# Performance work log

Hardware: AMD Instinct MI355X
Metric: run time of the kernel (lower is better)

The kernel has to match this reference:

```python
import jax, jax.numpy as jnp
import numpy as np

B, SQ, SKV = 4, 2048, 2048
INPUT_DIM, EMBED_DIM, NUM_HEADS = 1024, 1024, 16
HEAD_DIM = EMBED_DIM // NUM_HEADS


def setup_inputs() -> dict:
    key = jax.random.key(0)
    kq, kc, kwkv, kwo = jax.random.split(key, 4)
    # xavier-uniform style scale for weights
    def xavier(k, shape):
        fan_in, fan_out = shape
        lim = jnp.sqrt(6.0 / (fan_in + fan_out))
        return jax.random.uniform(k, shape, jnp.float32, -lim, lim)
    return {
        "q": jax.random.normal(kq, (B, SQ, EMBED_DIM), jnp.float32),
        "c": jax.random.normal(kc, (B, SKV, INPUT_DIM), jnp.float32),
        "W_kv": xavier(kwkv, (INPUT_DIM, 2 * EMBED_DIM)),
        "b_kv": jnp.zeros((2 * EMBED_DIM,), jnp.float32),
        "W_o": xavier(kwo, (EMBED_DIM, EMBED_DIM)),
        "b_o": jnp.zeros((EMBED_DIM,), jnp.float32),
    }


def reference(q, c, W_kv, b_kv, W_o, b_o):
    Bc, Skv, _ = c.shape
    Bq, Sq, embed_dim = q.shape
    # KV projection from context: [B, Skv, 2*embed_dim]
    kv = c @ W_kv + b_kv
    kv = kv.reshape(Bc, Skv, NUM_HEADS, 2 * HEAD_DIM).transpose(0, 2, 1, 3)  # [B,H,Skv,2*hd]
    k, v = jnp.split(kv, 2, axis=-1)  # each [B,H,Skv,hd]
    # q is pre-projected; just split into heads
    qh = q.reshape(Bq, Sq, NUM_HEADS, HEAD_DIM).transpose(0, 2, 1, 3)  # [B,H,Sq,hd]
    scale = 1.0 / jnp.sqrt(jnp.asarray(HEAD_DIM, q.dtype))
    logits = jnp.einsum("bhqd,bhkd->bhqk", qh, k) * scale  # [B,H,Sq,Skv]
    attn = jax.nn.softmax(logits, axis=-1)
    values = jnp.einsum("bhqk,bhkd->bhqd", attn, v)  # [B,H,Sq,hd]
    values = values.transpose(0, 2, 1, 3).reshape(Bc, Sq, embed_dim)
    out = values @ W_o + b_o
    return out
```

## Files before the change

### kernel.cpp

```cpp
#include <hip/hip_runtime.h>

typedef __bf16 bf16x8 __attribute__((ext_vector_type(8)));
typedef float f32x4 __attribute__((ext_vector_type(4)));
typedef unsigned short u16;
typedef unsigned short u16x4 __attribute__((ext_vector_type(4)));
typedef unsigned short u16x8 __attribute__((ext_vector_type(8)));

#define DEVFN __device__ __forceinline__

DEVFN u16 f32_to_bf16(float f) {
  unsigned int u = __float_as_uint(f);
  u += 0x7FFFu + ((u >> 16) & 1u);
  return (u16)(u >> 16);
}

DEVFN u16 f32_to_bf16_fast(float f) {
  return (u16)((__float_as_uint(f) + 0x8000u) >> 16);
}

DEVFN void load_lds16(const void* g, void* l) {
  __builtin_amdgcn_global_load_lds(
      (__attribute__((address_space(1))) void*)g,
      (__attribute__((address_space(3))) void*)l,
      16, 0, 0);
}


__global__ void cvt_c_kernel(const float* __restrict__ in, u16* __restrict__ out) {
  int i = blockIdx.x * 256 + threadIdx.x;
  const float4* p = (const float4*)in + (size_t)i * 2;
  float4 a = p[0], b = p[1];
  u16x8 o;
  o[0] = f32_to_bf16(a.x); o[1] = f32_to_bf16(a.y);
  o[2] = f32_to_bf16(a.z); o[3] = f32_to_bf16(a.w);
  o[4] = f32_to_bf16(b.x); o[5] = f32_to_bf16(b.y);
  o[6] = f32_to_bf16(b.z); o[7] = f32_to_bf16(b.w);
  *(u16x8*)(out + (size_t)i * 8) = o;
}

__global__ void cvt_q_kernel(const float* __restrict__ in, u16* __restrict__ out) {
  const float SC = 0.125f * 1.44269504088896f;
  int i = blockIdx.x * 256 + threadIdx.x;
  int dc = i & 7, sx = (i >> 3) & 2047, h = (i >> 14) & 15, b = i >> 18;
  const float4* p = (const float4*)(in + ((size_t)(b * 2048 + sx)) * 1024 + h * 64 + dc * 8);
  float4 a = p[0], bb = p[1];
  u16x8 o;
  o[0] = f32_to_bf16(a.x * SC);  o[1] = f32_to_bf16(a.y * SC);
  o[2] = f32_to_bf16(a.z * SC);  o[3] = f32_to_bf16(a.w * SC);
  o[4] = f32_to_bf16(bb.x * SC); o[5] = f32_to_bf16(bb.y * SC);
  o[6] = f32_to_bf16(bb.z * SC); o[7] = f32_to_bf16(bb.w * SC);
  *(u16x8*)(out + (size_t)i * 8) = o;
}

__global__ void transpose_w_kernel(const float* __restrict__ in, u16* __restrict__ out, int N) {
  __shared__ u16 T[64 * 72];
  const int tid = threadIdx.x;
  const int n0 = blockIdx.x * 64, k0 = blockIdx.y * 64;
#pragma unroll
  for (int p = 0; p < 4; ++p) {
    int l = p * 256 + tid;
    int k = l >> 4, nc = l & 15;
    const float4 v = *(const float4*)(in + (size_t)(k0 + k) * N + n0 + nc * 4);
    T[(nc * 4 + 0) * 72 + k] = f32_to_bf16(v.x);
    T[(nc * 4 + 1) * 72 + k] = f32_to_bf16(v.y);
    T[(nc * 4 + 2) * 72 + k] = f32_to_bf16(v.z);
    T[(nc * 4 + 3) * 72 + k] = f32_to_bf16(v.w);
  }
  __syncthreads();
#pragma unroll
  for (int p = 0; p < 2; ++p) {
    int u = p * 256 + tid;
    int n = u >> 3, kc = u & 7;
    u16x8 o = *(const u16x8*)(T + n * 72 + kc * 8);
    *(u16x8*)(out + (size_t)(n0 + n) * 1024 + k0 + kc * 8) = o;
  }
}

__global__ void transpose_v_kernel(const u16* __restrict__ Vp, u16* __restrict__ Vt) {
  __shared__ u16 T[64 * 136];
  const int tid = threadIdx.x;
  const int kt = blockIdx.x;
  const int bh = blockIdx.y;
  const int kv0 = kt * 128;
#pragma unroll
  for (int p = 0; p < 4; ++p) {
    int l = p * 256 + tid;
    int kv = l >> 3, dc = l & 7;
    u16x8 v = *(const u16x8*)(Vp + ((size_t)bh * 2048 + kv0 + kv) * 64 + dc * 8);
#pragma unroll
    for (int j = 0; j < 8; ++j) T[(dc * 8 + j) * 136 + kv] = v[j];
  }
  __syncthreads();
#pragma unroll
  for (int p = 0; p < 4; ++p) {
    int u = p * 256 + tid;
    int d = u >> 4, kc = u & 15;
    u16x8 o = *(const u16x8*)(T + d * 136 + kc * 8);
    *(u16x8*)(Vt + ((size_t)bh * 64 + d) * 2048 + kv0 + kc * 8) = o;
  }
}

template <int MODE>
__global__ __launch_bounds__(256, 2) void gemm128(
    const u16* __restrict__ A, const u16* __restrict__ Bt,
    const float* __restrict__ bias,
    u16* __restrict__ outK, u16* __restrict__ outV,
    float* __restrict__ outF, int K) {
  __shared__ u16 As[128 * 64];
  __shared__ u16 Bs[128 * 64];
  const int tid = threadIdx.x;
  const int lane = tid & 63, w = tid >> 6, quad = lane >> 4, l15 = lane & 15;
  const int wm = w & 1, wn = w >> 1;
  const int tn = blockIdx.x, tm = blockIdx.y;
  const u16* Ab = A + (size_t)tm * 128 * K;
  const u16* Bb = Bt + (size_t)tn * 128 * K;

  const f32x4 zero4 = {0.f, 0.f, 0.f, 0.f};
  f32x4 acc[4][4];
#pragma unroll
  for (int mi = 0; mi < 4; ++mi)
#pragma unroll
    for (int ni = 0; ni < 4; ++ni) acc[mi][ni] = zero4;

  for (int k0 = 0; k0 < K; k0 += 64) {
#pragma unroll
    for (int p = 0; p < 4; ++p) {
      int l = p * 256 + tid;
      int r = l >> 3, dc = l & 7;
      int go = r * K + k0 + ((dc ^ (r & 7)) * 8);
      int lb = (p * 256 + (tid & 192)) * 8;
      load_lds16(Ab + go, As + lb);
      load_lds16(Bb + go, Bs + lb);
    }
    __syncthreads();
#pragma unroll
    for (int kk = 0; kk < 2; ++kk) {
      bf16x8 av[4], bv[4];
#pragma unroll
      for (int i = 0; i < 4; ++i) {
        int sw = ((kk * 4 + quad) ^ (l15 & 7)) * 8;
        av[i] = *(const bf16x8*)(As + (wm * 64 + i * 16 + l15) * 64 + sw);
        bv[i] = *(const bf16x8*)(Bs + (wn * 64 + i * 16 + l15) * 64 + sw);
      }
#pragma unroll
      for (int mi = 0; mi < 4; ++mi)
#pragma unroll
        for (int ni = 0; ni < 4; ++ni)
          acc[mi][ni] = __builtin_amdgcn_mfma_f32_16x16x32_bf16(av[mi], bv[ni], acc[mi][ni], 0, 0, 0);
    }
    __syncthreads();
  }

#pragma unroll
  for (int ni = 0; ni < 4; ++ni) {
    const int n = tn * 128 + wn * 64 + ni * 16 + l15;
    const float bb = bias[n];
#pragma unroll
    for (int mi = 0; mi < 4; ++mi) {
#pragma unroll
      for (int r = 0; r < 4; ++r) {
        const int m = tm * 128 + wm * 64 + mi * 16 + quad * 4 + r;
        float val = acc[mi][ni][r] + bb;
        if (MODE == 0) {
          int h = n >> 7, rr = n & 127;
          int b = m >> 11, sx = m & 2047;
          u16* dst = (rr < 64) ? outK : outV;
          dst[((size_t)(b * 16 + h) * 2048 + sx) * 64 + (rr & 63)] = f32_to_bf16(val);
        } else {
          outF[(size_t)m * 1024 + n] = val;
        }
      }
    }
  }
}

#define PSTR 40

__global__ __launch_bounds__(256, 3) void flash_kernel(
    const u16* __restrict__ Qh,
    const u16* __restrict__ Kp,
    const u16* __restrict__ Vt,
    u16* __restrict__ Opk) {
  __shared__ u16 Ks[128 * 64];
  __shared__ u16 Vts[64 * 128];
  __shared__ u16 Ps[4][32 * PSTR];
  __shared__ float lbuf[4][32];

  const int tid = threadIdx.x;
  const int lane = tid & 63, w = tid >> 6, quad = lane >> 4, l15 = lane & 15;
  const int qt = blockIdx.x, bh = blockIdx.y;
  const int q0 = qt * 128;

  const u16* qbase = Qh + ((size_t)bh * 2048 + q0) * 64;
  const u16* kbase = Kp + (size_t)bh * 2048 * 64;
  const u16* vbase = Vt + (size_t)bh * 64 * 2048;

#pragma unroll
  for (int p = 0; p < 4; ++p) {
    int l = p * 256 + tid;
    int qq = l >> 3, dc = l & 7;
    load_lds16(qbase + qq * 64 + ((dc ^ (qq & 7)) * 8), Ks + (p * 256 + (tid & 192)) * 8);
  }
  __syncthreads();
  bf16x8 bq[2][2];
#pragma unroll
  for (int qi = 0; qi < 2; ++qi)
#pragma unroll
    for (int kc = 0; kc < 2; ++kc)
      bq[qi][kc] = *(const bf16x8*)(Ks + (w * 32 + qi * 16 + l15) * 64 +
                                    (((kc * 4 + quad) ^ (l15 & 7)) * 8));
  __syncthreads();

  const f32x4 zero4 = {0.f, 0.f, 0.f, 0.f};
  f32x4 oacc[2][4];
  f32x4 lsumv[2] = {zero4, zero4};
#pragma unroll
  for (int qi = 0; qi < 2; ++qi)
#pragma unroll
    for (int di = 0; di < 4; ++di) oacc[qi][di] = zero4;

  u16* myP = &Ps[w][0];

  for (int t = 0; t < 16; ++t) {
    const int kv0 = t * 128;
#pragma unroll
    for (int p = 0; p < 4; ++p) {
      int l = p * 256 + tid;
      int kv = l >> 3, dc = l & 7;
      load_lds16(kbase + (kv0 + kv) * 64 + ((dc ^ (kv & 7)) * 8), Ks + (p * 256 + (tid & 192)) * 8);
    }
#pragma unroll
    for (int p = 0; p < 4; ++p) {
      int l = p * 256 + tid;
      int d = l >> 4, dc = l & 15;
      load_lds16(vbase + (size_t)d * 2048 + kv0 + ((dc ^ (d & 15)) * 8),
                 Vts + (p * 256 + (tid & 192)) * 8);
    }
    __syncthreads();

#pragma unroll
    for (int c = 0; c < 4; ++c) {
      f32x4 s[2][2];
#pragma unroll
      for (int k2 = 0; k2 < 2; ++k2)
#pragma unroll
        for (int qi = 0; qi < 2; ++qi) s[k2][qi] = zero4;
#pragma unroll
      for (int kc = 0; kc < 2; ++kc) {
        const int sw = ((kc * 4 + quad) ^ (l15 & 7)) * 8;
        bf16x8 ak0 = *(const bf16x8*)(Ks + ((c * 2 + 0) * 16 + l15) * 64 + sw);
        bf16x8 ak1 = *(const bf16x8*)(Ks + ((c * 2 + 1) * 16 + l15) * 64 + sw);
        s[0][0] = __builtin_amdgcn_mfma_f32_16x16x32_bf16(ak0, bq[0][kc], s[0][0], 0, 0, 0);
        s[0][1] = __builtin_amdgcn_mfma_f32_16x16x32_bf16(ak0, bq[1][kc], s[0][1], 0, 0, 0);
        s[1][0] = __builtin_amdgcn_mfma_f32_16x16x32_bf16(ak1, bq[0][kc], s[1][0], 0, 0, 0);
        s[1][1] = __builtin_amdgcn_mfma_f32_16x16x32_bf16(ak1, bq[1][kc], s[1][1], 0, 0, 0);
      }

#pragma unroll
      for (int qi = 0; qi < 2; ++qi) {
#pragma unroll
        for (int k2 = 0; k2 < 2; ++k2) {
          u16x4 pk;
          f32x4 pv;
#pragma unroll
          for (int r = 0; r < 4; ++r) {
            pv[r] = __builtin_amdgcn_exp2f(s[k2][qi][r]);
            pk[r] = f32_to_bf16_fast(pv[r]);
          }
          lsumv[qi] += pv;
          *(u16x4*)(myP + (qi * 16 + l15) * PSTR + k2 * 16 + quad * 4) = pk;
        }
      }

      bf16x8 ap0 = *(const bf16x8*)(myP + (0 * 16 + l15) * PSTR + quad * 8);
      bf16x8 ap1 = *(const bf16x8*)(myP + (1 * 16 + l15) * PSTR + quad * 8);
#pragma unroll
      for (int di = 0; di < 4; ++di) {
        bf16x8 bv = *(const bf16x8*)(Vts + (di * 16 + l15) * 128 + (((c * 4 + quad) ^ l15) * 8));
        oacc[0][di] = __builtin_amdgcn_mfma_f32_16x16x32_bf16(ap0, bv, oacc[0][di], 0, 0, 0);
        oacc[1][di] = __builtin_amdgcn_mfma_f32_16x16x32_bf16(ap1, bv, oacc[1][di], 0, 0, 0);
      }
    }
    __syncthreads();
  }

  float lt[2];
#pragma unroll
  for (int qi = 0; qi < 2; ++qi) {
    float v = lsumv[qi][0] + lsumv[qi][1] + lsumv[qi][2] + lsumv[qi][3];
    v += __shfl_xor(v, 16);
    v += __shfl_xor(v, 32);
    lt[qi] = v;
  }
  if (lane < 16) {
    lbuf[w][lane] = lt[0];
    lbuf[w][16 + lane] = lt[1];
  }

  const int b = bh >> 4, h = bh & 15;
#pragma unroll
  for (int qi = 0; qi < 2; ++qi) {
#pragma unroll
    for (int r = 0; r < 4; ++r) {
      float linv = 1.0f / lbuf[w][qi * 16 + quad * 4 + r];
      int row = q0 + w * 32 + qi * 16 + quad * 4 + r;
      u16* dst = Opk + ((size_t)(b * 2048 + row)) * 1024 + h * 64;
#pragma unroll
      for (int di = 0; di < 4; ++di)
        dst[di * 16 + l15] = f32_to_bf16(oacc[qi][di][r] * linv);
    }
  }
}


extern "C" void kernel_launch(void* const* d_in, const int* in_sizes, int n_in,
                              void* d_out, int out_size, void* d_ws, size_t ws_size,
                              hipStream_t stream) {
  const float* q   = (const float*)d_in[0];
  const float* c   = (const float*)d_in[1];
  const float* Wkv = (const float*)d_in[2];
  const float* bkv = (const float*)d_in[3];
  const float* Wo  = (const float*)d_in[4];
  const float* bo  = (const float*)d_in[5];
  float* out = (float*)d_out;
  char* ws = (char*)d_ws;

  u16* c_bf = (u16*)(ws + 0);
  u16* qh   = (u16*)(ws + 16777216);
  u16* Wkvt = (u16*)(ws + 33554432);
  u16* Wot  = (u16*)(ws + 37748736);
  u16* KpB  = (u16*)(ws + 39845888);
  u16* VpB  = (u16*)(ws + 56623104);
  u16* VtB  = (u16*)(ws + 73400320);
  u16* Opk  = c_bf;

  cvt_c_kernel<<<4096, 256, 0, stream>>>(c, c_bf);
  cvt_q_kernel<<<4096, 256, 0, stream>>>(q, qh);
  transpose_w_kernel<<<dim3(32, 16), 256, 0, stream>>>(Wkv, Wkvt, 2048);
  transpose_w_kernel<<<dim3(16, 16), 256, 0, stream>>>(Wo, Wot, 1024);
  gemm128<0><<<dim3(16, 64), 256, 0, stream>>>(c_bf, Wkvt, bkv, KpB, VpB, nullptr, 1024);
  transpose_v_kernel<<<dim3(16, 64), 256, 0, stream>>>(VpB, VtB);
  flash_kernel<<<dim3(16, 64), 256, 0, stream>>>(qh, KpB, VtB, Opk);
  gemm128<1><<<dim3(8, 64), 256, 0, stream>>>(Opk, Wot, bo, nullptr, nullptr, out, 1024);
}
```

Before: 302.2 us.

## Fuse V transpose into KV GEMM, merge convert kernels, shrink flash query tile

Merges the c and q bf16 conversion kernels into one launch. The KV GEMM epilogue now transposes V through shared memory and writes it directly in the [d, kv] layout, which removes the separate transpose kernel and the V staging buffer. The flash kernel drops from 128 to 64 query rows per block, with 16 rows per wave loaded straight from global memory. It uses 2048 blocks in a swizzled head-grouped order and raises the occupancy bound to 4, trading more K/V re-reads for better occupancy and L2 locality.

```diff
diff --git a/kernel.cpp b/kernel.cpp
--- a/kernel.cpp
+++ b/kernel.cpp
@@ -25,35 +25,36 @@
       16, 0, 0);
 }
 
-
-__global__ void cvt_c_kernel(const float* __restrict__ in, u16* __restrict__ out) {
-  int i = blockIdx.x * 256 + threadIdx.x;
-  const float4* p = (const float4*)in + (size_t)i * 2;
-  float4 a = p[0], b = p[1];
-  u16x8 o;
-  o[0] = f32_to_bf16(a.x); o[1] = f32_to_bf16(a.y);
-  o[2] = f32_to_bf16(a.z); o[3] = f32_to_bf16(a.w);
-  o[4] = f32_to_bf16(b.x); o[5] = f32_to_bf16(b.y);
-  o[6] = f32_to_bf16(b.z); o[7] = f32_to_bf16(b.w);
-  *(u16x8*)(out + (size_t)i * 8) = o;
-}
-
-__global__ void cvt_q_kernel(const float* __restrict__ in, u16* __restrict__ out) {
-  const float SC = 0.125f * 1.44269504088896f;
-  int i = blockIdx.x * 256 + threadIdx.x;
-  int dc = i & 7, sx = (i >> 3) & 2047, h = (i >> 14) & 15, b = i >> 18;
-  const float4* p = (const float4*)(in + ((size_t)(b * 2048 + sx)) * 1024 + h * 64 + dc * 8);
-  float4 a = p[0], bb = p[1];
-  u16x8 o;
-  o[0] = f32_to_bf16(a.x * SC);  o[1] = f32_to_bf16(a.y * SC);
-  o[2] = f32_to_bf16(a.z * SC);  o[3] = f32_to_bf16(a.w * SC);
-  o[4] = f32_to_bf16(bb.x * SC); o[5] = f32_to_bf16(bb.y * SC);
-  o[6] = f32_to_bf16(bb.z * SC); o[7] = f32_to_bf16(bb.w * SC);
-  *(u16x8*)(out + (size_t)i * 8) = o;
+__global__ void cvt_cq_kernel(const float* __restrict__ c, const float* __restrict__ q,
+                              u16* __restrict__ c_bf, u16* __restrict__ qh) {
+  const int bid = blockIdx.x;
+  if (bid < 4096) {
+    int i = bid * 256 + threadIdx.x;
+    const float4* p = (const float4*)c + (size_t)i * 2;
+    float4 a = p[0], b = p[1];
+    u16x8 o;
+    o[0] = f32_to_bf16(a.x); o[1] = f32_to_bf16(a.y);
+    o[2] = f32_to_bf16(a.z); o[3] = f32_to_bf16(a.w);
+    o[4] = f32_to_bf16(b.x); o[5] = f32_to_bf16(b.y);
+    o[6] = f32_to_bf16(b.z); o[7] = f32_to_bf16(b.w);
+    *(u16x8*)(c_bf + (size_t)i * 8) = o;
+  } else {
+    const float SC = 0.125f * 1.44269504088896f;
+    int i = (bid - 4096) * 256 + threadIdx.x;
+    int dc = i & 7, sx = (i >> 3) & 2047, h = (i >> 14) & 15, b = i >> 18;
+    const float4* p = (const float4*)(q + ((size_t)(b * 2048 + sx)) * 1024 + h * 64 + dc * 8);
+    float4 a = p[0], bb = p[1];
+    u16x8 o;
+    o[0] = f32_to_bf16(a.x * SC);  o[1] = f32_to_bf16(a.y * SC);
+    o[2] = f32_to_bf16(a.z * SC);  o[3] = f32_to_bf16(a.w * SC);
+    o[4] = f32_to_bf16(bb.x * SC); o[5] = f32_to_bf16(bb.y * SC);
+    o[6] = f32_to_bf16(bb.z * SC); o[7] = f32_to_bf16(bb.w * SC);
+    *(u16x8*)(qh + (size_t)i * 8) = o;
+  }
 }
 
 __global__ void transpose_w_kernel(const float* __restrict__ in, u16* __restrict__ out, int N) {
-  __shared__ u16 T[64 * 72];
+  __shared__ __align__(16) u16 T[64 * 72];
   const int tid = threadIdx.x;
   const int n0 = blockIdx.x * 64, k0 = blockIdx.y * 64;
 #pragma unroll
@@ -76,38 +77,15 @@
   }
 }
 
-__global__ void transpose_v_kernel(const u16* __restrict__ Vp, u16* __restrict__ Vt) {
-  __shared__ u16 T[64 * 136];
-  const int tid = threadIdx.x;
-  const int kt = blockIdx.x;
-  const int bh = blockIdx.y;
-  const int kv0 = kt * 128;
-#pragma unroll
-  for (int p = 0; p < 4; ++p) {
-    int l = p * 256 + tid;
-    int kv = l >> 3, dc = l & 7;
-    u16x8 v = *(const u16x8*)(Vp + ((size_t)bh * 2048 + kv0 + kv) * 64 + dc * 8);
-#pragma unroll
-    for (int j = 0; j < 8; ++j) T[(dc * 8 + j) * 136 + kv] = v[j];
-  }
-  __syncthreads();
-#pragma unroll
-  for (int p = 0; p < 4; ++p) {
-    int u = p * 256 + tid;
-    int d = u >> 4, kc = u & 15;
-    u16x8 o = *(const u16x8*)(T + d * 136 + kc * 8);
-    *(u16x8*)(Vt + ((size_t)bh * 64 + d) * 2048 + kv0 + kc * 8) = o;
-  }
-}
-
 template <int MODE>
 __global__ __launch_bounds__(256, 2) void gemm128(
     const u16* __restrict__ A, const u16* __restrict__ Bt,
     const float* __restrict__ bias,
     u16* __restrict__ outK, u16* __restrict__ outV,
     float* __restrict__ outF, int K) {
-  __shared__ u16 As[128 * 64];
-  __shared__ u16 Bs[128 * 64];
+  __shared__ __align__(16) u16 SMEM[2 * 128 * 64];
+  u16* As = SMEM;
+  u16* Bs = SMEM + 128 * 64;
   const int tid = threadIdx.x;
   const int lane = tid & 63, w = tid >> 6, quad = lane >> 4, l15 = lane & 15;
   const int wm = w & 1, wn = w >> 1;
@@ -151,73 +129,96 @@
     __syncthreads();
   }
 
-#pragma unroll
-  for (int ni = 0; ni < 4; ++ni) {
-    const int n = tn * 128 + wn * 64 + ni * 16 + l15;
-    const float bb = bias[n];
-#pragma unroll
-    for (int mi = 0; mi < 4; ++mi) {
-#pragma unroll
-      for (int r = 0; r < 4; ++r) {
-        const int m = tm * 128 + wm * 64 + mi * 16 + quad * 4 + r;
-        float val = acc[mi][ni][r] + bb;
-        if (MODE == 0) {
-          int h = n >> 7, rr = n & 127;
-          int b = m >> 11, sx = m & 2047;
-          u16* dst = (rr < 64) ? outK : outV;
-          dst[((size_t)(b * 16 + h) * 2048 + sx) * 64 + (rr & 63)] = f32_to_bf16(val);
-        } else {
-          outF[(size_t)m * 1024 + n] = val;
+  if (MODE == 0) {
+    const int h = tn;
+    const int b = tm >> 4;
+    const int sx0 = (tm & 15) * 128;
+    u16* VT = SMEM;
+    if (wn == 0) {
+#pragma unroll
+      for (int ni = 0; ni < 4; ++ni) {
+        const int d = ni * 16 + l15;
+        const float bb = bias[tn * 128 + d];
+#pragma unroll
+        for (int mi = 0; mi < 4; ++mi) {
+#pragma unroll
+          for (int r = 0; r < 4; ++r) {
+            const int sx = sx0 + wm * 64 + mi * 16 + quad * 4 + r;
+            outK[((size_t)(b * 16 + h) * 2048 + sx) * 64 + d] = f32_to_bf16(acc[mi][ni][r] + bb);
+          }
         }
       }
+    } else {
+#pragma unroll
+      for (int ni = 0; ni < 4; ++ni) {
+        const int d = ni * 16 + l15;
+        const float bb = bias[tn * 128 + 64 + d];
+#pragma unroll
+        for (int mi = 0; mi < 4; ++mi) {
+          u16x4 pk;
+#pragma unroll
+          for (int r = 0; r < 4; ++r) pk[r] = f32_to_bf16(acc[mi][ni][r] + bb);
+          *(u16x4*)(VT + d * 136 + wm * 64 + mi * 16 + quad * 4) = pk;
+        }
+      }
+    }
+    __syncthreads();
+    {
+      const int d = tid >> 2, ch = tid & 3;
+      u16* dst = outV + (((size_t)(b * 16 + h) * 64 + d) * 2048 + sx0 + ch * 32);
+      const u16* src = VT + d * 136 + ch * 32;
+#pragma unroll
+      for (int i = 0; i < 4; ++i)
+        *(u16x8*)(dst + i * 8) = *(const u16x8*)(src + i * 8);
+    }
+  } else {
+#pragma unroll
+    for (int ni = 0; ni < 4; ++ni) {
+      const int n = tn * 128 + wn * 64 + ni * 16 + l15;
+      const float bb = bias[n];
+#pragma unroll
+      for (int mi = 0; mi < 4; ++mi) {
+#pragma unroll
+        for (int r = 0; r < 4; ++r) {
+          const int m = tm * 128 + wm * 64 + mi * 16 + quad * 4 + r;
+          outF[(size_t)m * 1024 + n] = acc[mi][ni][r] + bb;
+        }
+      }
     }
   }
 }
 
 #define PSTR 40
 
-__global__ __launch_bounds__(256, 3) void flash_kernel(
+__global__ __launch_bounds__(256, 4) void flash_kernel(
     const u16* __restrict__ Qh,
     const u16* __restrict__ Kp,
     const u16* __restrict__ Vt,
     u16* __restrict__ Opk) {
-  __shared__ u16 Ks[128 * 64];
-  __shared__ u16 Vts[64 * 128];
-  __shared__ u16 Ps[4][32 * PSTR];
-  __shared__ float lbuf[4][32];
+  __shared__ __align__(16) u16 Ks[128 * 64];
+  __shared__ __align__(16) u16 Vts[64 * 128];
+  __shared__ __align__(16) u16 Ps[4][16 * PSTR];
+  __shared__ float lbuf[4][16];
 
   const int tid = threadIdx.x;
   const int lane = tid & 63, w = tid >> 6, quad = lane >> 4, l15 = lane & 15;
-  const int qt = blockIdx.x, bh = blockIdx.y;
-  const int q0 = qt * 128;
-
-  const u16* qbase = Qh + ((size_t)bh * 2048 + q0) * 64;
+  const int id = blockIdx.x;
+  const int bh = (id & 7) + 8 * (id >> 8);
+  const int qt = (id >> 3) & 31;
+  const int q0 = qt * 64;
+
   const u16* kbase = Kp + (size_t)bh * 2048 * 64;
   const u16* vbase = Vt + (size_t)bh * 64 * 2048;
 
-#pragma unroll
-  for (int p = 0; p < 4; ++p) {
-    int l = p * 256 + tid;
-    int qq = l >> 3, dc = l & 7;
-    load_lds16(qbase + qq * 64 + ((dc ^ (qq & 7)) * 8), Ks + (p * 256 + (tid & 192)) * 8);
-  }
-  __syncthreads();
-  bf16x8 bq[2][2];
-#pragma unroll
-  for (int qi = 0; qi < 2; ++qi)
-#pragma unroll
-    for (int kc = 0; kc < 2; ++kc)
-      bq[qi][kc] = *(const bf16x8*)(Ks + (w * 32 + qi * 16 + l15) * 64 +
-                                    (((kc * 4 + quad) ^ (l15 & 7)) * 8));
-  __syncthreads();
+  const u16* qrow = Qh + ((size_t)bh * 2048 + q0 + w * 16 + l15) * 64;
+  bf16x8 bq0 = *(const bf16x8*)(qrow + quad * 8);
+  bf16x8 bq1 = *(const bf16x8*)(qrow + 32 + quad * 8);
 
   const f32x4 zero4 = {0.f, 0.f, 0.f, 0.f};
-  f32x4 oacc[2][4];
-  f32x4 lsumv[2] = {zero4, zero4};
-#pragma unroll
-  for (int qi = 0; qi < 2; ++qi)
-#pragma unroll
-    for (int di = 0; di < 4; ++di) oacc[qi][di] = zero4;
+  f32x4 oacc[4];
+  f32x4 lsumv = zero4;
+#pragma unroll
+  for (int di = 0; di < 4; ++di) oacc[di] = zero4;
 
   u16* myP = &Ps[w][0];
 
@@ -240,75 +241,60 @@
 
 #pragma unroll
     for (int c = 0; c < 4; ++c) {
-      f32x4 s[2][2];
-#pragma unroll
-      for (int k2 = 0; k2 < 2; ++k2)
-#pragma unroll
-        for (int qi = 0; qi < 2; ++qi) s[k2][qi] = zero4;
-#pragma unroll
-      for (int kc = 0; kc < 2; ++kc) {
-        const int sw = ((kc * 4 + quad) ^ (l15 & 7)) * 8;
-        bf16x8 ak0 = *(const bf16x8*)(Ks + ((c * 2 + 0) * 16 + l15) * 64 + sw);
-        bf16x8 ak1 = *(const bf16x8*)(Ks + ((c * 2 + 1) * 16 + l15) * 64 + sw);
-        s[0][0] = __builtin_amdgcn_mfma_f32_16x16x32_bf16(ak0, bq[0][kc], s[0][0], 0, 0, 0);
-        s[0][1] = __builtin_amdgcn_mfma_f32_16x16x32_bf16(ak0, bq[1][kc], s[0][1], 0, 0, 0);
-        s[1][0] = __builtin_amdgcn_mfma_f32_16x16x32_bf16(ak1, bq[0][kc], s[1][0], 0, 0, 0);
-        s[1][1] = __builtin_amdgcn_mfma_f32_16x16x32_bf16(ak1, bq[1][kc], s[1][1], 0, 0, 0);
-      }
-
-#pragma unroll
-      for (int qi = 0; qi < 2; ++qi) {
-#pragma unroll
-        for (int k2 = 0; k2 < 2; ++k2) {
-          u16x4 pk;
-          f32x4 pv;
-#pragma unroll
-          for (int r = 0; r < 4; ++r) {
-            pv[r] = __builtin_amdgcn_exp2f(s[k2][qi][r]);
-            pk[r] = f32_to_bf16_fast(pv[r]);
-          }
-          lsumv[qi] += pv;
-          *(u16x4*)(myP + (qi * 16 + l15) * PSTR + k2 * 16 + quad * 4) = pk;
+      f32x4 s0 = zero4, s1 = zero4;
+      {
+        const int sw0 = (quad ^ (l15 & 7)) * 8;
+        bf16x8 ak0 = *(const bf16x8*)(Ks + ((c * 2 + 0) * 16 + l15) * 64 + sw0);
+        bf16x8 ak1 = *(const bf16x8*)(Ks + ((c * 2 + 1) * 16 + l15) * 64 + sw0);
+        s0 = __builtin_amdgcn_mfma_f32_16x16x32_bf16(ak0, bq0, s0, 0, 0, 0);
+        s1 = __builtin_amdgcn_mfma_f32_16x16x32_bf16(ak1, bq0, s1, 0, 0, 0);
+        const int sw1 = ((4 + quad) ^ (l15 & 7)) * 8;
+        ak0 = *(const bf16x8*)(Ks + ((c * 2 + 0) * 16 + l15) * 64 + sw1);
+        ak1 = *(const bf16x8*)(Ks + ((c * 2 + 1) * 16 + l15) * 64 + sw1);
+        s0 = __builtin_amdgcn_mfma_f32_16x16x32_bf16(ak0, bq1, s0, 0, 0, 0);
+        s1 = __builtin_amdgcn_mfma_f32_16x16x32_bf16(ak1, bq1, s1, 0, 0, 0);
+      }
+
+#pragma unroll
+      for (int k2 = 0; k2 < 2; ++k2) {
+        const f32x4& s = (k2 == 0) ? s0 : s1;
+        u16x4 pk;
+        f32x4 pv;
+#pragma unroll
+        for (int r = 0; r < 4; ++r) {
+          pv[r] = __builtin_amdgcn_exp2f(s[r]);
+          pk[r] = f32_to_bf16_fast(pv[r]);
         }
-      }
-
-      bf16x8 ap0 = *(const bf16x8*)(myP + (0 * 16 + l15) * PSTR + quad * 8);
-      bf16x8 ap1 = *(const bf16x8*)(myP + (1 * 16 + l15) * PSTR + quad * 8);
+        lsumv += pv;
+        *(u16x4*)(myP + l15 * PSTR + k2 * 16 + quad * 4) = pk;
+      }
+
+      bf16x8 ap = *(const bf16x8*)(myP + l15 * PSTR + quad * 8);
 #pragma unroll
       for (int di = 0; di < 4; ++di) {
         bf16x8 bv = *(const bf16x8*)(Vts + (di * 16 + l15) * 128 + (((c * 4 + quad) ^ l15) * 8));
-        oacc[0][di] = __builtin_amdgcn_mfma_f32_16x16x32_bf16(ap0, bv, oacc[0][di], 0, 0, 0);
-        oacc[1][di] = __builtin_amdgcn_mfma_f32_16x16x32_bf16(ap1, bv, oacc[1][di], 0, 0, 0);
-      }
-    }
-    __syncthreads();
-  }
-
-  float lt[2];
-#pragma unroll
-  for (int qi = 0; qi < 2; ++qi) {
-    float v = lsumv[qi][0] + lsumv[qi][1] + lsumv[qi][2] + lsumv[qi][3];
+        oacc[di] = __builtin_amdgcn_mfma_f32_16x16x32_bf16(ap, bv, oacc[di], 0, 0, 0);
+      }
+    }
+    __syncthreads();
+  }
+
+  {
+    float v = lsumv[0] + lsumv[1] + lsumv[2] + lsumv[3];
     v += __shfl_xor(v, 16);
     v += __shfl_xor(v, 32);
-    lt[qi] = v;
-  }
-  if (lane < 16) {
-    lbuf[w][lane] = lt[0];
-    lbuf[w][16 + lane] = lt[1];
+    if (lane < 16) lbuf[w][lane] = v;
   }
 
   const int b = bh >> 4, h = bh & 15;
 #pragma unroll
-  for (int qi = 0; qi < 2; ++qi) {
-#pragma unroll
-    for (int r = 0; r < 4; ++r) {
-      float linv = 1.0f / lbuf[w][qi * 16 + quad * 4 + r];
-      int row = q0 + w * 32 + qi * 16 + quad * 4 + r;
-      u16* dst = Opk + ((size_t)(b * 2048 + row)) * 1024 + h * 64;
-#pragma unroll
-      for (int di = 0; di < 4; ++di)
-        dst[di * 16 + l15] = f32_to_bf16(oacc[qi][di][r] * linv);
-    }
+  for (int r = 0; r < 4; ++r) {
+    float linv = 1.0f / lbuf[w][quad * 4 + r];
+    int row = q0 + w * 16 + quad * 4 + r;
+    u16* dst = Opk + ((size_t)(b * 2048 + row)) * 1024 + h * 64;
+#pragma unroll
+    for (int di = 0; di < 4; ++di)
+      dst[di * 16 + l15] = f32_to_bf16(oacc[di][r] * linv);
   }
 }
 
@@ -330,16 +316,13 @@
   u16* Wkvt = (u16*)(ws + 33554432);
   u16* Wot  = (u16*)(ws + 37748736);
   u16* KpB  = (u16*)(ws + 39845888);
-  u16* VpB  = (u16*)(ws + 56623104);
-  u16* VtB  = (u16*)(ws + 73400320);
+  u16* VtB  = (u16*)(ws + 56623104);
   u16* Opk  = c_bf;
 
-  cvt_c_kernel<<<4096, 256, 0, stream>>>(c, c_bf);
-  cvt_q_kernel<<<4096, 256, 0, stream>>>(q, qh);
+  cvt_cq_kernel<<<8192, 256, 0, stream>>>(c, q, c_bf, qh);
   transpose_w_kernel<<<dim3(32, 16), 256, 0, stream>>>(Wkv, Wkvt, 2048);
   transpose_w_kernel<<<dim3(16, 16), 256, 0, stream>>>(Wo, Wot, 1024);
-  gemm128<0><<<dim3(16, 64), 256, 0, stream>>>(c_bf, Wkvt, bkv, KpB, VpB, nullptr, 1024);
-  transpose_v_kernel<<<dim3(16, 64), 256, 0, stream>>>(VpB, VtB);
-  flash_kernel<<<dim3(16, 64), 256, 0, stream>>>(qh, KpB, VtB, Opk);
+  gemm128<0><<<dim3(16, 64), 256, 0, stream>>>(c_bf, Wkvt, bkv, KpB, VtB, nullptr, 1024);
+  flash_kernel<<<2048, 256, 0, stream>>>(qh, KpB, VtB, Opk);
   gemm128<1><<<dim3(8, 64), 256, 0, stream>>>(Opk, Wot, bo, nullptr, nullptr, out, 1024);
 }
```

After: 284.1 us. 6.0% less time.
